# Optimization experiments

Hardware: AMD Instinct MI355X
Metric: run time of the kernel (lower is better)

Reference implementation:

```python
import jax, jax.numpy as jnp
import numpy as np
from math import sqrt


def setup_inputs() -> dict:
    key = jax.random.key(0)
    kq, kk, kv = jax.random.split(key, 3)
    B, L, H, E = 4, 2048, 8, 64
    S, D = L, E
    return {
        "queries": jax.random.normal(kq, (B, L, H, E), dtype=jnp.float32),
        "keys": jax.random.normal(kk, (B, S, H, E), dtype=jnp.float32),
        "values": jax.random.normal(kv, (B, S, H, D), dtype=jnp.float32),
    }


def reference(queries, keys, values):
    # FullAttention with mask_flag=True (TriangularCausalMask), dropout p=0,
    # output_attention=False. scale = 1/sqrt(E).
    B, L, H, E = queries.shape
    S = keys.shape[1]
    scale = 1.0 / sqrt(E)
    # scores: [B, H, L, S]
    scores = jnp.einsum("blhe,bshe->bhls", queries, keys)
    # causal mask: positions s > l are masked (upper triangle above diagonal)
    causal = jnp.tril(jnp.ones((L, S), dtype=bool))  # True = keep
    neg_inf = jnp.finfo(scores.dtype).min
    scores = jnp.where(causal, scores, neg_inf)
    A = jax.nn.softmax(scale * scores, axis=-1)  # [B,H,L,S]
    # context: [B, L, H, D]
    V = jnp.einsum("bhls,bshd->blhd", A, values)
    return V
```

## Files before the change

### kernel.cpp

```cpp
#include <hip/hip_runtime.h>
#include <math.h>

#define BD 4
#define LD 2048
#define HD 8
#define ED 64
#define TQ 128
#define TK 64
#define RS (HD * ED)

typedef __attribute__((ext_vector_type(8))) _Float16 f16x8;
typedef __attribute__((ext_vector_type(4))) _Float16 f16x4;
typedef __attribute__((ext_vector_type(4))) float f32x4;
typedef __attribute__((ext_vector_type(4))) unsigned int u32x4;
typedef __attribute__((ext_vector_type(2))) unsigned int u32x2;
typedef unsigned int u32;
typedef unsigned long long u64;

__device__ inline u32 pkh(float a, float b) {
    return __builtin_bit_cast(u32, __builtin_amdgcn_cvt_pkrtz(a, b));
}
__device__ inline u64 pkh4(float a, float b, float c, float d) {
    return (u64)pkh(a, b) | ((u64)pkh(c, d) << 32);
}
__device__ inline int swz(int row, int bcol) {
    return row * 128 + ((((bcol >> 4) ^ row) & 7) << 4) + (bcol & 15);
}

__global__ __launch_bounds__(256, 2)
void fa_mfma_k16(const float* __restrict__ Q, const float* __restrict__ K,
                 const float* __restrict__ V, float* __restrict__ O) {
    __shared__ __align__(16) char smem[32768];

    const int t    = threadIdx.x;
    const int lane = t & 63;
    const int w    = t >> 6;
    const int m16  = lane & 15;
    const int quad = lane >> 4;

    const int b = blockIdx.x >> 3;
    const int h = blockIdx.x & 7;
    const int y   = (int)blockIdx.y;
    const int qtp = (y < 8) ? (15 - y) : (y - 8);
    const int q0  = qtp * TQ;
    const int kmax = 2 * qtp + 1;

    const int ks  = t >> 2;
    const int ke0 = (t & 3) << 2;
    const int vs0 = (t & 15) << 2;
    const int vd0 = (t >> 4) << 2;

    const float* Kbase = K + ((size_t)((b * LD + ks) * HD + h)) * ED + ke0;
    const float* Vbase = V + ((size_t)((b * LD + vs0) * HD + h)) * ED + vd0;

    const float qscale = 0.125f * 1.44269504088896340736f;
    f16x8 qf[2][2];
    #pragma unroll
    for (int sub = 0; sub < 2; ++sub) {
        const float* qrow =
            Q + ((size_t)((b * LD + q0 + (w << 5) + (sub << 4) + m16) * HD + h)) * ED;
        #pragma unroll
        for (int hf = 0; hf < 2; ++hf) {
            const float4 x = *(const float4*)(qrow + hf * 32 + quad * 8);
            const float4 y4 = *(const float4*)(qrow + hf * 32 + quad * 8 + 4);
            u32x4 p;
            p[0] = pkh(x.x * qscale, x.y * qscale);
            p[1] = pkh(x.z * qscale, x.w * qscale);
            p[2] = pkh(y4.x * qscale, y4.y * qscale);
            p[3] = pkh(y4.z * qscale, y4.w * qscale);
            qf[sub][hf] = __builtin_bit_cast(f16x8, p);
        }
    }

    f32x4 oacc[2][4];
    float l_i[2] = {0.0f, 0.0f};
    #pragma unroll
    for (int sub = 0; sub < 2; ++sub)
        #pragma unroll
        for (int nt = 0; nt < 4; ++nt) oacc[sub][nt] = (f32x4){0.f, 0.f, 0.f, 0.f};

    float4 kx[4], vx[4];
    {
        #pragma unroll
        for (int j = 0; j < 4; ++j) kx[j] = *(const float4*)(Kbase + 16 * j);
        #pragma unroll
        for (int r = 0; r < 4; ++r) vx[r] = *(const float4*)(Vbase + r * RS);
        char* wK = smem;
        char* wV = smem + 16384;
        #pragma unroll
        for (int j = 0; j < 4; ++j)
            *(u64*)(wK + swz(ks, 2 * (ke0 + 16 * j))) = pkh4(kx[j].x, kx[j].y, kx[j].z, kx[j].w);
        *(u64*)(wV + swz(vd0 + 0, 2 * vs0)) = pkh4(vx[0].x, vx[1].x, vx[2].x, vx[3].x);
        *(u64*)(wV + swz(vd0 + 1, 2 * vs0)) = pkh4(vx[0].y, vx[1].y, vx[2].y, vx[3].y);
        *(u64*)(wV + swz(vd0 + 2, 2 * vs0)) = pkh4(vx[0].z, vx[1].z, vx[2].z, vx[3].z);
        *(u64*)(wV + swz(vd0 + 3, 2 * vs0)) = pkh4(vx[0].w, vx[1].w, vx[2].w, vx[3].w);
    }
    __syncthreads();

    for (int kt = 0; kt <= kmax; ++kt) {
        char* rK = smem + ((kt & 1) << 13);
        char* rV = smem + 16384 + ((kt & 1) << 13);
        const bool pre = kt < kmax;

        if (pre) {
            const float* kp = Kbase + (size_t)(kt + 1) * (TK * RS);
            const float* vp = Vbase + (size_t)(kt + 1) * (TK * RS);
            #pragma unroll
            for (int j = 0; j < 4; ++j) kx[j] = *(const float4*)(kp + 16 * j);
            #pragma unroll
            for (int r = 0; r < 4; ++r) vx[r] = *(const float4*)(vp + r * RS);
        }

        const int offq = (2 * qtp - kt) * 64;
        if (offq + (w << 5) + 31 >= 0) {
            f32x4 sacc[2][4];
            #pragma unroll
            for (int kc = 0; kc < 4; ++kc) {
                const f16x8 kf0 = *(const f16x8*)(rK + swz(kc * 16 + m16, quad * 16));
                const f16x8 kf1 = *(const f16x8*)(rK + swz(kc * 16 + m16, 64 + quad * 16));
                #pragma unroll
                for (int sub = 0; sub < 2; ++sub) {
                    f32x4 z = {0.f, 0.f, 0.f, 0.f};
                    z = __builtin_amdgcn_mfma_f32_16x16x32_f16(kf0, qf[sub][0], z, 0, 0, 0);
                    z = __builtin_amdgcn_mfma_f32_16x16x32_f16(kf1, qf[sub][1], z, 0, 0, 0);
                    sacc[sub][kc] = z;
                }
            }

            if (offq < 64) {
                #pragma unroll
                for (int sub = 0; sub < 2; ++sub) {
                    const int ql = (w << 5) + (sub << 4) + m16 + offq;
                    #pragma unroll
                    for (int kc = 0; kc < 4; ++kc)
                        #pragma unroll
                        for (int i = 0; i < 4; ++i)
                            if (kc * 16 + quad * 4 + i > ql) sacc[sub][kc][i] = -INFINITY;
                }
            }

            f16x4 pf[2][4];
            #pragma unroll
            for (int sub = 0; sub < 2; ++sub) {
                #pragma unroll
                for (int kc = 0; kc < 4; ++kc) {
                    float p0 = __builtin_amdgcn_exp2f(sacc[sub][kc][0]);
                    float p1 = __builtin_amdgcn_exp2f(sacc[sub][kc][1]);
                    float p2 = __builtin_amdgcn_exp2f(sacc[sub][kc][2]);
                    float p3 = __builtin_amdgcn_exp2f(sacc[sub][kc][3]);
                    l_i[sub] += (p0 + p1) + (p2 + p3);
                    u32x2 pp;
                    pp[0] = pkh(p0, p1);
                    pp[1] = pkh(p2, p3);
                    pf[sub][kc] = __builtin_bit_cast(f16x4, pp);
                }
            }

            #pragma unroll
            for (int kc = 0; kc < 4; ++kc) {
                #pragma unroll
                for (int dt = 0; dt < 4; ++dt) {
                    const f16x4 vf = *(const f16x4*)
                        (rV + swz(dt * 16 + m16, 2 * (kc * 16 + quad * 4)));
                    oacc[0][dt] = __builtin_amdgcn_mfma_f32_16x16x16f16(vf, pf[0][kc], oacc[0][dt], 0, 0, 0);
                    oacc[1][dt] = __builtin_amdgcn_mfma_f32_16x16x16f16(vf, pf[1][kc], oacc[1][dt], 0, 0, 0);
                }
            }
        }

        if (pre) {
            char* wK = smem + ((kt & 1) ? 0 : 8192);
            char* wV = smem + 16384 + ((kt & 1) ? 0 : 8192);
            #pragma unroll
            for (int j = 0; j < 4; ++j)
                *(u64*)(wK + swz(ks, 2 * (ke0 + 16 * j))) = pkh4(kx[j].x, kx[j].y, kx[j].z, kx[j].w);
            *(u64*)(wV + swz(vd0 + 0, 2 * vs0)) = pkh4(vx[0].x, vx[1].x, vx[2].x, vx[3].x);
            *(u64*)(wV + swz(vd0 + 1, 2 * vs0)) = pkh4(vx[0].y, vx[1].y, vx[2].y, vx[3].y);
            *(u64*)(wV + swz(vd0 + 2, 2 * vs0)) = pkh4(vx[0].z, vx[1].z, vx[2].z, vx[3].z);
            *(u64*)(wV + swz(vd0 + 3, 2 * vs0)) = pkh4(vx[0].w, vx[1].w, vx[2].w, vx[3].w);
        }
        __syncthreads();
    }

    #pragma unroll
    for (int sub = 0; sub < 2; ++sub) {
        float l = l_i[sub];
        l += __shfl_xor(l, 16);
        l += __shfl_xor(l, 32);
        const float inv = 1.0f / l;
        float* orow =
            O + ((size_t)((b * LD + q0 + (w << 5) + (sub << 4) + m16) * HD + h)) * ED;
        #pragma unroll
        for (int dt = 0; dt < 4; ++dt) {
            float4 o;
            o.x = oacc[sub][dt][0] * inv;
            o.y = oacc[sub][dt][1] * inv;
            o.z = oacc[sub][dt][2] * inv;
            o.w = oacc[sub][dt][3] * inv;
            *(float4*)(orow + dt * 16 + quad * 4) = o;
        }
    }
}

extern "C" void kernel_launch(void* const* d_in, const int* in_sizes, int n_in,
                              void* d_out, int out_size, void* d_ws, size_t ws_size,
                              hipStream_t stream) {
    const float* Q = (const float*)d_in[0];
    const float* K = (const float*)d_in[1];
    const float* V = (const float*)d_in[2];
    float* O = (float*)d_out;
    dim3 grid(BD * HD, LD / TQ);
    fa_mfma_k16<<<grid, 256, 0, stream>>>(Q, K, V, O);
}
```

Measured before the change: 122.4 us.

## Split KV range across two blocks per query tile with combine kernel

Each query tile's causal KV range is split into two halves processed by separate blocks, which write unnormalized partial outputs and row sums to the workspace. A second kernel adds the partials and normalizes them. This doubles the grid to improve occupancy and load balance, and raises the launch bound to 4 blocks. In exchange it adds an extra kernel launch and extra global traffic for the partial outputs. It relies on the absence of max subtraction, so partials can be summed directly, and it only takes this path when a large enough workspace is provided.

```diff
diff --git a/kernel.cpp b/kernel.cpp
--- a/kernel.cpp
+++ b/kernel.cpp
@@ -27,9 +27,11 @@
     return row * 128 + ((((bcol >> 4) ^ row) & 7) << 4) + (bcol & 15);
 }
 
-__global__ __launch_bounds__(256, 2)
+template <bool SPLIT>
+__global__ __launch_bounds__(256, SPLIT ? 4 : 2)
 void fa_mfma_k16(const float* __restrict__ Q, const float* __restrict__ K,
-                 const float* __restrict__ V, float* __restrict__ O) {
+                 const float* __restrict__ V, float* __restrict__ O,
+                 float* __restrict__ O1, float* __restrict__ Lp) {
     __shared__ __align__(16) char smem[32768];
 
     const int t    = threadIdx.x;
@@ -41,17 +43,20 @@
     const int b = blockIdx.x >> 3;
     const int h = blockIdx.x & 7;
     const int y   = (int)blockIdx.y;
-    const int qtp = (y < 8) ? (15 - y) : (y - 8);
+    const int sp  = SPLIT ? (y >> 4) : 0;
+    const int yy  = SPLIT ? (y & 15) : y;
+    const int qtp = (yy < 8) ? (15 - yy) : (yy - 8);
     const int q0  = qtp * TQ;
-    const int kmax = 2 * qtp + 1;
+    const int len = SPLIT ? (qtp + 1) : (2 * qtp + 2);
+    const int k0  = sp * len;
 
     const int ks  = t >> 2;
     const int ke0 = (t & 3) << 2;
     const int vs0 = (t & 15) << 2;
     const int vd0 = (t >> 4) << 2;
 
-    const float* Kbase = K + ((size_t)((b * LD + ks) * HD + h)) * ED + ke0;
-    const float* Vbase = V + ((size_t)((b * LD + vs0) * HD + h)) * ED + vd0;
+    const float* Kbase = K + ((size_t)((b * LD + k0 * TK + ks) * HD + h)) * ED + ke0;
+    const float* Vbase = V + ((size_t)((b * LD + k0 * TK + vs0) * HD + h)) * ED + vd0;
 
     const float qscale = 0.125f * 1.44269504088896340736f;
     f16x8 qf[2][2];
@@ -97,14 +102,15 @@
     }
     __syncthreads();
 
-    for (int kt = 0; kt <= kmax; ++kt) {
-        char* rK = smem + ((kt & 1) << 13);
-        char* rV = smem + 16384 + ((kt & 1) << 13);
-        const bool pre = kt < kmax;
+    for (int it = 0; it < len; ++it) {
+        const int kt = k0 + it;
+        char* rK = smem + ((it & 1) << 13);
+        char* rV = smem + 16384 + ((it & 1) << 13);
+        const bool pre = it < len - 1;
 
         if (pre) {
-            const float* kp = Kbase + (size_t)(kt + 1) * (TK * RS);
-            const float* vp = Vbase + (size_t)(kt + 1) * (TK * RS);
+            const float* kp = Kbase + (size_t)(it + 1) * (TK * RS);
+            const float* vp = Vbase + (size_t)(it + 1) * (TK * RS);
             #pragma unroll
             for (int j = 0; j < 4; ++j) kx[j] = *(const float4*)(kp + 16 * j);
             #pragma unroll
@@ -169,8 +175,8 @@
         }
 
         if (pre) {
-            char* wK = smem + ((kt & 1) ? 0 : 8192);
-            char* wV = smem + 16384 + ((kt & 1) ? 0 : 8192);
+            char* wK = smem + ((it & 1) ? 0 : 8192);
+            char* wV = smem + 16384 + ((it & 1) ? 0 : 8192);
             #pragma unroll
             for (int j = 0; j < 4; ++j)
                 *(u64*)(wK + swz(ks, 2 * (ke0 + 16 * j))) = pkh4(kx[j].x, kx[j].y, kx[j].z, kx[j].w);
@@ -187,19 +193,50 @@
         float l = l_i[sub];
         l += __shfl_xor(l, 16);
         l += __shfl_xor(l, 32);
-        const float inv = 1.0f / l;
-        float* orow =
-            O + ((size_t)((b * LD + q0 + (w << 5) + (sub << 4) + m16) * HD + h)) * ED;
-        #pragma unroll
-        for (int dt = 0; dt < 4; ++dt) {
-            float4 o;
-            o.x = oacc[sub][dt][0] * inv;
-            o.y = oacc[sub][dt][1] * inv;
-            o.z = oacc[sub][dt][2] * inv;
-            o.w = oacc[sub][dt][3] * inv;
-            *(float4*)(orow + dt * 16 + quad * 4) = o;
-        }
-    }
+        const int qrow = q0 + (w << 5) + (sub << 4) + m16;
+        if constexpr (SPLIT) {
+            float* orow = (sp ? O1 : O) + ((size_t)((b * LD + qrow) * HD + h)) * ED;
+            #pragma unroll
+            for (int dt = 0; dt < 4; ++dt) {
+                float4 o;
+                o.x = oacc[sub][dt][0];
+                o.y = oacc[sub][dt][1];
+                o.z = oacc[sub][dt][2];
+                o.w = oacc[sub][dt][3];
+                *(float4*)(orow + dt * 16 + quad * 4) = o;
+            }
+            if (lane < 16)
+                Lp[(size_t)sp * (BD * LD * HD) + ((size_t)(b * LD + qrow)) * HD + h] = l;
+        } else {
+            const float inv = 1.0f / l;
+            float* orow = O + ((size_t)((b * LD + qrow) * HD + h)) * ED;
+            #pragma unroll
+            for (int dt = 0; dt < 4; ++dt) {
+                float4 o;
+                o.x = oacc[sub][dt][0] * inv;
+                o.y = oacc[sub][dt][1] * inv;
+                o.z = oacc[sub][dt][2] * inv;
+                o.w = oacc[sub][dt][3] * inv;
+                *(float4*)(orow + dt * 16 + quad * 4) = o;
+            }
+        }
+    }
+}
+
+__global__ __launch_bounds__(256)
+void fa_combine(float* __restrict__ O, const float* __restrict__ O1,
+                const float* __restrict__ Lp) {
+    const size_t idx = (size_t)blockIdx.x * 256 + threadIdx.x;
+    const size_t row = idx >> 4;
+    const float inv = 1.0f / (Lp[row] + Lp[(size_t)(BD * LD * HD) + row]);
+    const float4 a = *((const float4*)O + idx);
+    const float4 c = *((const float4*)O1 + idx);
+    float4 o;
+    o.x = (a.x + c.x) * inv;
+    o.y = (a.y + c.y) * inv;
+    o.z = (a.z + c.z) * inv;
+    o.w = (a.w + c.w) * inv;
+    *((float4*)O + idx) = o;
 }
 
 extern "C" void kernel_launch(void* const* d_in, const int* in_sizes, int n_in,
@@ -209,6 +246,20 @@
     const float* K = (const float*)d_in[1];
     const float* V = (const float*)d_in[2];
     float* O = (float*)d_out;
-    dim3 grid(BD * HD, LD / TQ);
-    fa_mfma_k16<<<grid, 256, 0, stream>>>(Q, K, V, O);
-}
+
+    const size_t oelems = (size_t)BD * LD * HD * ED;
+    const size_t lelems = (size_t)2 * BD * LD * HD;
+    const size_t need   = (oelems + lelems) * sizeof(float);
+
+    if (d_ws != nullptr && ws_size >= need) {
+        float* O1 = (float*)d_ws;
+        float* Lp = (float*)d_ws + oelems;
+        dim3 g1(BD * HD, 32);
+        fa_mfma_k16<true><<<g1, 256, 0, stream>>>(Q, K, V, O, O1, Lp);
+        const int nb = (int)(oelems / 4 / 256);
+        fa_combine<<<dim3(nb), 256, 0, stream>>>(O, O1, Lp);
+    } else {
+        dim3 grid(BD * HD, LD / TQ);
+        fa_mfma_k16<false><<<grid, 256, 0, stream>>>(Q, K, V, O, nullptr, nullptr);
+    }
+}
```

New measurement: 221.9 us. +81.4%, slower.

## Halve query tile to 64 rows and raise occupancy with reordered causal scheduling

Applied to the files above, without the earlier changes.

Shrinks the query tile from 128 to 64 rows, so each wave handles one 16-row sub-tile and the grid doubles to 1024 blocks. Launch bounds now request 4 blocks per SM, and a new block-to-tile mapping interleaves long and short causal tiles for load balance. The partial-diagonal skipping logic is simplified because only the last key tile needs masking. More blocks reload the same K/V, roughly doubling K/V global traffic and fp16 conversion work per query row, in exchange for more parallelism and latency hiding.

```diff
diff --git a/kernel.cpp b/kernel.cpp
--- a/kernel.cpp
+++ b/kernel.cpp
@@ -5,7 +5,7 @@
 #define LD 2048
 #define HD 8
 #define ED 64
-#define TQ 128
+#define TQ 64
 #define TK 64
 #define RS (HD * ED)
 
@@ -27,8 +27,8 @@
     return row * 128 + ((((bcol >> 4) ^ row) & 7) << 4) + (bcol & 15);
 }
 
-__global__ __launch_bounds__(256, 2)
-void fa_mfma_k16(const float* __restrict__ Q, const float* __restrict__ K,
+__global__ __launch_bounds__(256, 4)
+void fa_mfma_q64(const float* __restrict__ Q, const float* __restrict__ K,
                  const float* __restrict__ V, float* __restrict__ O) {
     __shared__ __align__(16) char smem[32768];
 
@@ -40,10 +40,13 @@
 
     const int b = blockIdx.x >> 3;
     const int h = blockIdx.x & 7;
-    const int y   = (int)blockIdx.y;
-    const int qtp = (y < 8) ? (15 - y) : (y - 8);
-    const int q0  = qtp * TQ;
-    const int kmax = 2 * qtp + 1;
+    const int y  = (int)blockIdx.y;
+    const int r  = y & 7;
+    const int c  = y >> 3;
+    const int qt = (c == 0) ? (31 - r) : (c == 1) ? (r + 8)
+                 : (c == 2) ? (23 - r) : r;
+    const int q0  = qt * TQ;
+    const int len = qt + 1;
 
     const int ks  = t >> 2;
     const int ke0 = (t & 3) << 2;
@@ -54,37 +57,34 @@
     const float* Vbase = V + ((size_t)((b * LD + vs0) * HD + h)) * ED + vd0;
 
     const float qscale = 0.125f * 1.44269504088896340736f;
-    f16x8 qf[2][2];
-    #pragma unroll
-    for (int sub = 0; sub < 2; ++sub) {
+    f16x8 qf[2];
+    {
         const float* qrow =
-            Q + ((size_t)((b * LD + q0 + (w << 5) + (sub << 4) + m16) * HD + h)) * ED;
+            Q + ((size_t)((b * LD + q0 + (w << 4) + m16) * HD + h)) * ED;
         #pragma unroll
         for (int hf = 0; hf < 2; ++hf) {
-            const float4 x = *(const float4*)(qrow + hf * 32 + quad * 8);
+            const float4 x  = *(const float4*)(qrow + hf * 32 + quad * 8);
             const float4 y4 = *(const float4*)(qrow + hf * 32 + quad * 8 + 4);
             u32x4 p;
             p[0] = pkh(x.x * qscale, x.y * qscale);
             p[1] = pkh(x.z * qscale, x.w * qscale);
             p[2] = pkh(y4.x * qscale, y4.y * qscale);
             p[3] = pkh(y4.z * qscale, y4.w * qscale);
-            qf[sub][hf] = __builtin_bit_cast(f16x8, p);
-        }
-    }
-
-    f32x4 oacc[2][4];
-    float l_i[2] = {0.0f, 0.0f};
+            qf[hf] = __builtin_bit_cast(f16x8, p);
+        }
+    }
+
+    f32x4 oacc[4];
+    float l_i = 0.0f;
     #pragma unroll
-    for (int sub = 0; sub < 2; ++sub)
-        #pragma unroll
-        for (int nt = 0; nt < 4; ++nt) oacc[sub][nt] = (f32x4){0.f, 0.f, 0.f, 0.f};
+    for (int nt = 0; nt < 4; ++nt) oacc[nt] = (f32x4){0.f, 0.f, 0.f, 0.f};
 
     float4 kx[4], vx[4];
     {
         #pragma unroll
         for (int j = 0; j < 4; ++j) kx[j] = *(const float4*)(Kbase + 16 * j);
         #pragma unroll
-        for (int r = 0; r < 4; ++r) vx[r] = *(const float4*)(Vbase + r * RS);
+        for (int rr = 0; rr < 4; ++rr) vx[rr] = *(const float4*)(Vbase + rr * RS);
         char* wK = smem;
         char* wV = smem + 16384;
         #pragma unroll
@@ -97,10 +97,10 @@
     }
     __syncthreads();
 
-    for (int kt = 0; kt <= kmax; ++kt) {
+    for (int kt = 0; kt < len; ++kt) {
         char* rK = smem + ((kt & 1) << 13);
         char* rV = smem + 16384 + ((kt & 1) << 13);
-        const bool pre = kt < kmax;
+        const bool pre = kt < len - 1;
 
         if (pre) {
             const float* kp = Kbase + (size_t)(kt + 1) * (TK * RS);
@@ -108,63 +108,50 @@
             #pragma unroll
             for (int j = 0; j < 4; ++j) kx[j] = *(const float4*)(kp + 16 * j);
             #pragma unroll
-            for (int r = 0; r < 4; ++r) vx[r] = *(const float4*)(vp + r * RS);
-        }
-
-        const int offq = (2 * qtp - kt) * 64;
-        if (offq + (w << 5) + 31 >= 0) {
-            f32x4 sacc[2][4];
-            #pragma unroll
-            for (int kc = 0; kc < 4; ++kc) {
-                const f16x8 kf0 = *(const f16x8*)(rK + swz(kc * 16 + m16, quad * 16));
-                const f16x8 kf1 = *(const f16x8*)(rK + swz(kc * 16 + m16, 64 + quad * 16));
+            for (int rr = 0; rr < 4; ++rr) vx[rr] = *(const float4*)(vp + rr * RS);
+        }
+
+        f32x4 sacc[4];
+        #pragma unroll
+        for (int kc = 0; kc < 4; ++kc) {
+            const f16x8 kf0 = *(const f16x8*)(rK + swz(kc * 16 + m16, quad * 16));
+            const f16x8 kf1 = *(const f16x8*)(rK + swz(kc * 16 + m16, 64 + quad * 16));
+            f32x4 z = {0.f, 0.f, 0.f, 0.f};
+            z = __builtin_amdgcn_mfma_f32_16x16x32_f16(kf0, qf[0], z, 0, 0, 0);
+            z = __builtin_amdgcn_mfma_f32_16x16x32_f16(kf1, qf[1], z, 0, 0, 0);
+            sacc[kc] = z;
+        }
+
+        if (kt == qt) {
+            const int ql = (w << 4) + m16;
+            #pragma unroll
+            for (int kc = 0; kc < 4; ++kc)
                 #pragma unroll
-                for (int sub = 0; sub < 2; ++sub) {
-                    f32x4 z = {0.f, 0.f, 0.f, 0.f};
-                    z = __builtin_amdgcn_mfma_f32_16x16x32_f16(kf0, qf[sub][0], z, 0, 0, 0);
-                    z = __builtin_amdgcn_mfma_f32_16x16x32_f16(kf1, qf[sub][1], z, 0, 0, 0);
-                    sacc[sub][kc] = z;
-                }
-            }
-
-            if (offq < 64) {
-                #pragma unroll
-                for (int sub = 0; sub < 2; ++sub) {
-                    const int ql = (w << 5) + (sub << 4) + m16 + offq;
-                    #pragma unroll
-                    for (int kc = 0; kc < 4; ++kc)
-                        #pragma unroll
-                        for (int i = 0; i < 4; ++i)
-                            if (kc * 16 + quad * 4 + i > ql) sacc[sub][kc][i] = -INFINITY;
-                }
-            }
-
-            f16x4 pf[2][4];
-            #pragma unroll
-            for (int sub = 0; sub < 2; ++sub) {
-                #pragma unroll
-                for (int kc = 0; kc < 4; ++kc) {
-                    float p0 = __builtin_amdgcn_exp2f(sacc[sub][kc][0]);
-                    float p1 = __builtin_amdgcn_exp2f(sacc[sub][kc][1]);
-                    float p2 = __builtin_amdgcn_exp2f(sacc[sub][kc][2]);
-                    float p3 = __builtin_amdgcn_exp2f(sacc[sub][kc][3]);
-                    l_i[sub] += (p0 + p1) + (p2 + p3);
-                    u32x2 pp;
-                    pp[0] = pkh(p0, p1);
-                    pp[1] = pkh(p2, p3);
-                    pf[sub][kc] = __builtin_bit_cast(f16x4, pp);
-                }
-            }
-
-            #pragma unroll
-            for (int kc = 0; kc < 4; ++kc) {
-                #pragma unroll
-                for (int dt = 0; dt < 4; ++dt) {
-                    const f16x4 vf = *(const f16x4*)
-                        (rV + swz(dt * 16 + m16, 2 * (kc * 16 + quad * 4)));
-                    oacc[0][dt] = __builtin_amdgcn_mfma_f32_16x16x16f16(vf, pf[0][kc], oacc[0][dt], 0, 0, 0);
-                    oacc[1][dt] = __builtin_amdgcn_mfma_f32_16x16x16f16(vf, pf[1][kc], oacc[1][dt], 0, 0, 0);
-                }
+                for (int i = 0; i < 4; ++i)
+                    if (kc * 16 + quad * 4 + i > ql) sacc[kc][i] = -INFINITY;
+        }
+
+        f16x4 pf[4];
+        #pragma unroll
+        for (int kc = 0; kc < 4; ++kc) {
+            float p0 = __builtin_amdgcn_exp2f(sacc[kc][0]);
+            float p1 = __builtin_amdgcn_exp2f(sacc[kc][1]);
+            float p2 = __builtin_amdgcn_exp2f(sacc[kc][2]);
+            float p3 = __builtin_amdgcn_exp2f(sacc[kc][3]);
+            l_i += (p0 + p1) + (p2 + p3);
+            u32x2 pp;
+            pp[0] = pkh(p0, p1);
+            pp[1] = pkh(p2, p3);
+            pf[kc] = __builtin_bit_cast(f16x4, pp);
+        }
+
+        #pragma unroll
+        for (int kc = 0; kc < 4; ++kc) {
+            #pragma unroll
+            for (int dt = 0; dt < 4; ++dt) {
+                const f16x4 vf = *(const f16x4*)
+                    (rV + swz(dt * 16 + m16, 2 * (kc * 16 + quad * 4)));
+                oacc[dt] = __builtin_amdgcn_mfma_f32_16x16x16f16(vf, pf[kc], oacc[dt], 0, 0, 0);
             }
         }
 
@@ -182,21 +169,20 @@
         __syncthreads();
     }
 
-    #pragma unroll
-    for (int sub = 0; sub < 2; ++sub) {
-        float l = l_i[sub];
+    {
+        float l = l_i;
         l += __shfl_xor(l, 16);
         l += __shfl_xor(l, 32);
         const float inv = 1.0f / l;
         float* orow =
-            O + ((size_t)((b * LD + q0 + (w << 5) + (sub << 4) + m16) * HD + h)) * ED;
+            O + ((size_t)((b * LD + q0 + (w << 4) + m16) * HD + h)) * ED;
         #pragma unroll
         for (int dt = 0; dt < 4; ++dt) {
             float4 o;
-            o.x = oacc[sub][dt][0] * inv;
-            o.y = oacc[sub][dt][1] * inv;
-            o.z = oacc[sub][dt][2] * inv;
-            o.w = oacc[sub][dt][3] * inv;
+            o.x = oacc[dt][0] * inv;
+            o.y = oacc[dt][1] * inv;
+            o.z = oacc[dt][2] * inv;
+            o.w = oacc[dt][3] * inv;
             *(float4*)(orow + dt * 16 + quad * 4) = o;
         }
     }
@@ -209,6 +195,6 @@
     const float* K = (const float*)d_in[1];
     const float* V = (const float*)d_in[2];
     float* O = (float*)d_out;
-    dim3 grid(BD * HD, LD / TQ);
-    fa_mfma_k16<<<grid, 256, 0, stream>>>(Q, K, V, O);
-}
+    dim3 grid(BD * HD, 32);
+    fa_mfma_q64<<<grid, 256, 0, stream>>>(Q, K, V, O);
+}
```

After: 124.0 us. About the same (+1.4%).

## Split KV tiles across two wave groups per block and merge partial outputs

Applied to the files above, without the earlier changes.

Doubles the block to 512 threads. Two groups of four waves each process alternating 64-key tiles for the same 128-query tile, which halves the serial KV loop length per block. Each group has its own double-buffered K/V shared memory, 64KB in total. At the end, group 1's partial accumulators and row sums go through shared memory and group 0 adds them and normalises. Because no running max is used, the merge is a plain sum. It also adds s_setprio around the MFMA sections. The larger shared-memory footprint and the extra merge step can lower occupancy.

```diff
diff --git a/kernel.cpp b/kernel.cpp
--- a/kernel.cpp
+++ b/kernel.cpp
@@ -27,48 +27,54 @@
     return row * 128 + ((((bcol >> 4) ^ row) & 7) << 4) + (bcol & 15);
 }
 
-__global__ __launch_bounds__(256, 2)
-void fa_mfma_k16(const float* __restrict__ Q, const float* __restrict__ K,
-                 const float* __restrict__ V, float* __restrict__ O) {
-    __shared__ __align__(16) char smem[32768];
+__global__ __launch_bounds__(512, 4)
+void fa_mfma_kpar(const float* __restrict__ Q, const float* __restrict__ K,
+                  const float* __restrict__ V, float* __restrict__ O) {
+    __shared__ __align__(16) char smem[65536];
 
     const int t    = threadIdx.x;
     const int lane = t & 63;
     const int w    = t >> 6;
+    const int wr   = w & 3;
+    const int p    = w >> 2;
     const int m16  = lane & 15;
     const int quad = lane >> 4;
 
     const int b = blockIdx.x >> 3;
     const int h = blockIdx.x & 7;
-    const int y   = (int)blockIdx.y;
-    const int qtp = (y < 8) ? (15 - y) : (y - 8);
-    const int q0  = qtp * TQ;
-    const int kmax = 2 * qtp + 1;
-
-    const int ks  = t >> 2;
-    const int ke0 = (t & 3) << 2;
-    const int vs0 = (t & 15) << 2;
-    const int vd0 = (t >> 4) << 2;
-
-    const float* Kbase = K + ((size_t)((b * LD + ks) * HD + h)) * ED + ke0;
-    const float* Vbase = V + ((size_t)((b * LD + vs0) * HD + h)) * ED + vd0;
+    const int y  = (int)blockIdx.y;
+    const int qt = (y < 8) ? (15 - y) : (y - 8);
+    const int q0 = qt * TQ;
+    const int nIter = qt + 1;
+
+    const int tt  = t & 255;
+    const int ks  = tt >> 2;
+    const int ke0 = (tt & 3) << 2;
+    const int vs0 = (tt & 15) << 2;
+    const int vd0 = (tt >> 4) << 2;
+
+    const float* Kbase = K + ((size_t)((b * LD + p * TK + ks) * HD + h)) * ED + ke0;
+    const float* Vbase = V + ((size_t)((b * LD + p * TK + vs0) * HD + h)) * ED + vd0;
+
+    char* const myK = smem + p * 16384;
+    char* const myV = smem + 32768 + p * 16384;
 
     const float qscale = 0.125f * 1.44269504088896340736f;
     f16x8 qf[2][2];
     #pragma unroll
     for (int sub = 0; sub < 2; ++sub) {
         const float* qrow =
-            Q + ((size_t)((b * LD + q0 + (w << 5) + (sub << 4) + m16) * HD + h)) * ED;
+            Q + ((size_t)((b * LD + q0 + (wr << 5) + (sub << 4) + m16) * HD + h)) * ED;
         #pragma unroll
         for (int hf = 0; hf < 2; ++hf) {
-            const float4 x = *(const float4*)(qrow + hf * 32 + quad * 8);
+            const float4 x  = *(const float4*)(qrow + hf * 32 + quad * 8);
             const float4 y4 = *(const float4*)(qrow + hf * 32 + quad * 8 + 4);
-            u32x4 p;
-            p[0] = pkh(x.x * qscale, x.y * qscale);
-            p[1] = pkh(x.z * qscale, x.w * qscale);
-            p[2] = pkh(y4.x * qscale, y4.y * qscale);
-            p[3] = pkh(y4.z * qscale, y4.w * qscale);
-            qf[sub][hf] = __builtin_bit_cast(f16x8, p);
+            u32x4 pk;
+            pk[0] = pkh(x.x * qscale, x.y * qscale);
+            pk[1] = pkh(x.z * qscale, x.w * qscale);
+            pk[2] = pkh(y4.x * qscale, y4.y * qscale);
+            pk[3] = pkh(y4.z * qscale, y4.w * qscale);
+            qf[sub][hf] = __builtin_bit_cast(f16x8, pk);
         }
     }
 
@@ -84,36 +90,36 @@
         #pragma unroll
         for (int j = 0; j < 4; ++j) kx[j] = *(const float4*)(Kbase + 16 * j);
         #pragma unroll
-        for (int r = 0; r < 4; ++r) vx[r] = *(const float4*)(Vbase + r * RS);
-        char* wK = smem;
-        char* wV = smem + 16384;
+        for (int rr = 0; rr < 4; ++rr) vx[rr] = *(const float4*)(Vbase + rr * RS);
         #pragma unroll
         for (int j = 0; j < 4; ++j)
-            *(u64*)(wK + swz(ks, 2 * (ke0 + 16 * j))) = pkh4(kx[j].x, kx[j].y, kx[j].z, kx[j].w);
-        *(u64*)(wV + swz(vd0 + 0, 2 * vs0)) = pkh4(vx[0].x, vx[1].x, vx[2].x, vx[3].x);
-        *(u64*)(wV + swz(vd0 + 1, 2 * vs0)) = pkh4(vx[0].y, vx[1].y, vx[2].y, vx[3].y);
-        *(u64*)(wV + swz(vd0 + 2, 2 * vs0)) = pkh4(vx[0].z, vx[1].z, vx[2].z, vx[3].z);
-        *(u64*)(wV + swz(vd0 + 3, 2 * vs0)) = pkh4(vx[0].w, vx[1].w, vx[2].w, vx[3].w);
+            *(u64*)(myK + swz(ks, 2 * (ke0 + 16 * j))) = pkh4(kx[j].x, kx[j].y, kx[j].z, kx[j].w);
+        *(u64*)(myV + swz(vd0 + 0, 2 * vs0)) = pkh4(vx[0].x, vx[1].x, vx[2].x, vx[3].x);
+        *(u64*)(myV + swz(vd0 + 1, 2 * vs0)) = pkh4(vx[0].y, vx[1].y, vx[2].y, vx[3].y);
+        *(u64*)(myV + swz(vd0 + 2, 2 * vs0)) = pkh4(vx[0].z, vx[1].z, vx[2].z, vx[3].z);
+        *(u64*)(myV + swz(vd0 + 3, 2 * vs0)) = pkh4(vx[0].w, vx[1].w, vx[2].w, vx[3].w);
     }
     __syncthreads();
 
-    for (int kt = 0; kt <= kmax; ++kt) {
-        char* rK = smem + ((kt & 1) << 13);
-        char* rV = smem + 16384 + ((kt & 1) << 13);
-        const bool pre = kt < kmax;
+    for (int it = 0; it < nIter; ++it) {
+        const int kt = 2 * it + p;
+        char* rK = myK + ((it & 1) << 13);
+        char* rV = myV + ((it & 1) << 13);
+        const bool pre = it < qt;
 
         if (pre) {
-            const float* kp = Kbase + (size_t)(kt + 1) * (TK * RS);
-            const float* vp = Vbase + (size_t)(kt + 1) * (TK * RS);
+            const float* kp = Kbase + (size_t)(it + 1) * (2 * TK * RS);
+            const float* vp = Vbase + (size_t)(it + 1) * (2 * TK * RS);
             #pragma unroll
             for (int j = 0; j < 4; ++j) kx[j] = *(const float4*)(kp + 16 * j);
             #pragma unroll
-            for (int r = 0; r < 4; ++r) vx[r] = *(const float4*)(vp + r * RS);
-        }
-
-        const int offq = (2 * qtp - kt) * 64;
-        if (offq + (w << 5) + 31 >= 0) {
+            for (int rr = 0; rr < 4; ++rr) vx[rr] = *(const float4*)(vp + rr * RS);
+        }
+
+        const int offq = (2 * qt - kt) * 64;
+        if (offq + (wr << 5) + 31 >= 0) {
             f32x4 sacc[2][4];
+            __builtin_amdgcn_s_setprio(1);
             #pragma unroll
             for (int kc = 0; kc < 4; ++kc) {
                 const f16x8 kf0 = *(const f16x8*)(rK + swz(kc * 16 + m16, quad * 16));
@@ -126,11 +132,12 @@
                     sacc[sub][kc] = z;
                 }
             }
+            __builtin_amdgcn_s_setprio(0);
 
             if (offq < 64) {
                 #pragma unroll
                 for (int sub = 0; sub < 2; ++sub) {
-                    const int ql = (w << 5) + (sub << 4) + m16 + offq;
+                    const int ql = (wr << 5) + (sub << 4) + m16 + offq;
                     #pragma unroll
                     for (int kc = 0; kc < 4; ++kc)
                         #pragma unroll
@@ -156,6 +163,7 @@
                 }
             }
 
+            __builtin_amdgcn_s_setprio(1);
             #pragma unroll
             for (int kc = 0; kc < 4; ++kc) {
                 #pragma unroll
@@ -166,11 +174,12 @@
                     oacc[1][dt] = __builtin_amdgcn_mfma_f32_16x16x16f16(vf, pf[1][kc], oacc[1][dt], 0, 0, 0);
                 }
             }
+            __builtin_amdgcn_s_setprio(0);
         }
 
         if (pre) {
-            char* wK = smem + ((kt & 1) ? 0 : 8192);
-            char* wV = smem + 16384 + ((kt & 1) ? 0 : 8192);
+            char* wK = myK + ((it & 1) ? 0 : 8192);
+            char* wV = myV + ((it & 1) ? 0 : 8192);
             #pragma unroll
             for (int j = 0; j < 4; ++j)
                 *(u64*)(wK + swz(ks, 2 * (ke0 + 16 * j))) = pkh4(kx[j].x, kx[j].y, kx[j].z, kx[j].w);
@@ -182,22 +191,44 @@
         __syncthreads();
     }
 
-    #pragma unroll
-    for (int sub = 0; sub < 2; ++sub) {
-        float l = l_i[sub];
-        l += __shfl_xor(l, 16);
-        l += __shfl_xor(l, 32);
-        const float inv = 1.0f / l;
-        float* orow =
-            O + ((size_t)((b * LD + q0 + (w << 5) + (sub << 4) + m16) * HD + h)) * ED;
-        #pragma unroll
-        for (int dt = 0; dt < 4; ++dt) {
-            float4 o;
-            o.x = oacc[sub][dt][0] * inv;
-            o.y = oacc[sub][dt][1] * inv;
-            o.z = oacc[sub][dt][2] * inv;
-            o.w = oacc[sub][dt][3] * inv;
-            *(float4*)(orow + dt * 16 + quad * 4) = o;
+    {
+        char* eo  = smem;
+        float* el = (float*)(smem + 32768);
+        const int erow = (wr << 6) + lane;
+        if (p == 1) {
+            #pragma unroll
+            for (int sub = 0; sub < 2; ++sub) {
+                el[erow * 2 + sub] = l_i[sub];
+                #pragma unroll
+                for (int dt = 0; dt < 4; ++dt)
+                    *(f32x4*)(eo + swz(erow, 16 * ((sub << 2) + dt))) = oacc[sub][dt];
+            }
+        }
+        __syncthreads();
+        if (p == 0) {
+            #pragma unroll
+            for (int sub = 0; sub < 2; ++sub) {
+                l_i[sub] += el[erow * 2 + sub];
+                #pragma unroll
+                for (int dt = 0; dt < 4; ++dt)
+                    oacc[sub][dt] += *(const f32x4*)(eo + swz(erow, 16 * ((sub << 2) + dt)));
+
+                float l = l_i[sub];
+                l += __shfl_xor(l, 16);
+                l += __shfl_xor(l, 32);
+                const float inv = 1.0f / l;
+                float* orow =
+                    O + ((size_t)((b * LD + q0 + (wr << 5) + (sub << 4) + m16) * HD + h)) * ED;
+                #pragma unroll
+                for (int dt = 0; dt < 4; ++dt) {
+                    float4 o;
+                    o.x = oacc[sub][dt][0] * inv;
+                    o.y = oacc[sub][dt][1] * inv;
+                    o.z = oacc[sub][dt][2] * inv;
+                    o.w = oacc[sub][dt][3] * inv;
+                    *(float4*)(orow + dt * 16 + quad * 4) = o;
+                }
+            }
         }
     }
 }
@@ -209,6 +240,6 @@
     const float* K = (const float*)d_in[1];
     const float* V = (const float*)d_in[2];
     float* O = (float*)d_out;
-    dim3 grid(BD * HD, LD / TQ);
-    fa_mfma_k16<<<grid, 256, 0, stream>>>(Q, K, V, O);
-}
+    dim3 grid(BD * HD, 16);
+    fa_mfma_kpar<<<grid, 512, 0, stream>>>(Q, K, V, O);
+}
```

Result: slower. 190.9 us (+56.0%).
